# Kernel tuning notes

Hardware: AMD Instinct MI355X
Metric: run time of the kernel (lower is better)

Reference implementation:

```python
import jax, jax.numpy as jnp
import numpy as np
from jax import lax

R = 2            # search_range
S = 2 * R + 1    # window extent per axis
NCH = S ** 3     # output channels (125)


def _offset_table():
    # Loop order matches the original triple loop (i over H, j over W, h over D).
    # Channel index (S*i + S*j + h) may be negative -> Python negative indexing,
    starts, chans = [], []
    for i in range(-R, R + 1):          # H shift
        for j in range(-R, R + 1):      # W shift
            for h in range(-R, R + 1):  # D shift
                # out[a] = sum_c x1[a] * x2[a - shift]; padded start = R - shift
                starts.append((R - h, R - i, R - j))
                chans.append((S * i + S * j + h) % NCH)
    src = np.full(NCH, -1, dtype=np.int64)
    for t, c in enumerate(chans):
        src[c] = t
    return np.asarray(starts, np.int32), src


def setup_inputs() -> dict:
    key = jax.random.key(0)
    k1, k2 = jax.random.split(key)
    B, C, D, H, W = 2, 64, 32, 64, 64
    x1 = jax.random.normal(k1, (B, C, D, H, W), dtype=jnp.float32)
    x2 = jax.random.normal(k2, (B, C, D, H, W), dtype=jnp.float32)
    return {"x1": x1, "x2": x2}


def reference(x1, x2):
    B, C, D, H, W = x1.shape
    starts_np, src_np = _offset_table()
    starts = jnp.asarray(starts_np)                          # [NCH, 3]
    # zero-pad x2 so every shifted window is a static-size slice
    x2p = jnp.pad(x2, ((0, 0), (0, 0), (R, R), (R, R), (R, R)))

    def corr(off):
        x2s = lax.dynamic_slice(x2p, (0, 0, off[0], off[1], off[2]),
                                (B, C, D, H, W))
        return jnp.einsum('bcdhw,bcdhw->bdhw', x1, x2s)

    corrs = lax.map(corr, starts)                            # [NCH, B, D, H, W]
    src = jnp.asarray(src_np)
    written = (src >= 0)[:, None, None, None, None]
    cv = jnp.where(written, corrs[jnp.clip(src, 0)], jnp.float32(0.0))
    return jnp.transpose(cv, (1, 0, 2, 3, 4)) / NCH          # [B, NCH, D, H, W]
```

## Files before the change

kernel.cpp:

```cpp
#include <hip/hip_runtime.h>

#define B_ 2
#define C_ 64
#define D_ 32
#define H_ 64
#define W_ 64
#define NCH 125
#define HW_ 4096
#define DHW_ 131072
#define CDHW_ 8388608

#define TROWS 8
#define TBUF (TROWS * W_)
#define WREG (3 * TBUF)

__device__ __attribute__((aligned(16))) const float g_zero[4] = {0.f, 0.f, 0.f, 0.f};

__device__ __forceinline__ void glds16(const float* g, float* l) {
    __builtin_amdgcn_global_load_lds(
        (const __attribute__((address_space(1))) void*)g,
        (__attribute__((address_space(3))) void*)l, 16, 0, 0);
}

__global__ __launch_bounds__(128, 5) void cv_all(const float* __restrict__ x1,
                                                 const float* __restrict__ x2,
                                                 float* __restrict__ out)
{
    __shared__ __align__(16) float lds[4 + 2 * WREG + 4];

    const int tid  = threadIdx.y * 16 + threadIdx.x;
    const int lane = tid & 63;
    const int w    = tid >> 6;
    const int tx   = lane & 15;
    const int lr0  = lane >> 4;

    const int lin     = blockIdx.x;
    const int logical = (lin & 7) * 320 + (lin >> 3);
    const int bz   = logical % 10;
    const int rest = logical / 10;
    const int y0   = (rest & 7) * 8;
    const int d    = rest >> 3;
    const int b    = bz / 5;
    const int hi   = bz - b * 5;
    const int hh   = hi - 2;
    const int y0w  = y0 + 4 * w;
    const int y    = y0w + lr0;
    const int x    = tx * 4;
    const int zd   = d - hh;
    const bool zok = (zd >= 0) && (zd < D_);

    const float* x2b = x2 + (size_t)b * CDHW_ + (size_t)(zok ? zd : 0) * HW_;
    const int q   = lane & 15;
    const int grA = y0w - 2 + (lane >> 4);
    const int grB = y0w + 2 + (lane >> 4);
    const bool vA = zok && (grA >= 0);
    const bool vB = zok && (grB < H_);
    const float* pA = vA ? (x2b + grA * W_ + 4 * q) : g_zero;
    const float* pB = vB ? (x2b + grB * W_ + 4 * q) : g_zero;
    const int sA = vA ? DHW_ : 0;
    const int sB = vB ? DHW_ : 0;

    const int wbase = 4 + w * WREG;
    const float* p1 = x1 + (size_t)b * CDHW_ + (size_t)d * HW_ + (y * W_ + x);

    float* obz = out + (size_t)b * NCH * DHW_ + (size_t)(23 + hi * 16) * DHW_
                     + (size_t)d * HW_ + (y * W_ + x);
    const float4 zero4 = make_float4(0.f, 0.f, 0.f, 0.f);

    glds16(pA, lds + wbase);
    glds16(pB, lds + wbase + TBUF / 2);
    float4 a0 = *(const float4*)p1;
    pA += sA; pB += sB;

    float acc[9][4];
#pragma unroll
    for (int k = 0; k < 9; ++k)
#pragma unroll
        for (int j = 0; j < 4; ++j) acc[k][j] = 0.f;

    const bool lo_edge = (tx == 0);
    const bool hi_edge = (tx == 15);

#pragma unroll 2
    for (int c = 0; c < C_; ++c) {
        float* dst = lds + wbase + ((c + 1) % 3) * TBUF;
        glds16(pA, dst);
        glds16(pB, dst + TBUF / 2);
        float4 a1 = *(const float4*)(p1 + (size_t)((c + 1) & 63) * DHW_);
        if (c < 62) { pA += sA; pB += sB; }

        asm volatile("s_waitcnt vmcnt(3)" ::: "memory");

        const float* Bb = lds + wbase + (c % 3) * TBUF;
        const float4 a = a0;
        float2 k0A, k0B;
#pragma unroll
        for (int k = 0; k < 5; ++k) {
            const float* pr = Bb + (lr0 + k) * W_ + x;
            const float2 cA = *(const float2*)(pr + 2);
            float2 cB = *(const float2*)(pr + 4);
            cB.x = hi_edge ? 0.f : cB.x;
            cB.y = hi_edge ? 0.f : cB.y;
            if (k == 0) { k0A = cA; k0B = cB; }
            const int ai = 4 - k;
            acc[ai][0] += a.x * cA.x;
            acc[ai][1] += a.y * cA.y;
            acc[ai][2] += a.z * cB.x;
            acc[ai][3] += a.w * cB.y;
        }
        {
            const float* pr = Bb + lr0 * W_ + x;
            float2 rlA = *(const float2*)(pr - 2);
            const float2 rlB = *(const float2*)(pr);
            rlA.x = lo_edge ? 0.f : rlA.x;
            rlA.y = lo_edge ? 0.f : rlA.y;
            const float r8[8] = {rlA.x, rlA.y, rlB.x, rlB.y,
                                 k0A.x, k0A.y, k0B.x, k0B.y};
#pragma unroll
            for (int s = 1; s <= 4; ++s) {
                const int ai = s + 4;
                acc[ai][0] += a.x * r8[4 - s];
                acc[ai][1] += a.y * r8[5 - s];
                acc[ai][2] += a.z * r8[6 - s];
                acc[ai][3] += a.w * r8[7 - s];
            }
        }
        a0 = a1;

        if ((c & 3) == 0)
            *(float4*)(obz + (size_t)(c >> 2) * DHW_) = zero4;
    }

    float* ob = out + (size_t)b * NCH * DHW_ + (size_t)d * HW_ + (y * W_ + x);
    const float inv = 1.0f / 125.0f;
#pragma unroll
    for (int k = 0; k < 9; ++k) {
        const int s = k - 4;
        int ch = 5 * s + hh;
        ch = (ch % NCH + NCH) % NCH;
        float4 v;
        v.x = acc[k][0] * inv;
        v.y = acc[k][1] * inv;
        v.z = acc[k][2] * inv;
        v.w = acc[k][3] * inv;
        *(float4*)(ob + (size_t)ch * DHW_) = v;
    }
}

extern "C" void kernel_launch(void* const* d_in, const int* in_sizes, int n_in,
                              void* d_out, int out_size, void* d_ws, size_t ws_size,
                              hipStream_t stream) {
    const float* x1 = (const float*)d_in[0];
    const float* x2 = (const float*)d_in[1];
    float* out = (float*)d_out;
    cv_all<<<dim3(2560, 1, 1), dim3(16, 8, 1), 0, stream>>>(x1, x2, out);
}
```

Before: 269.4 us.

## Replace direct global-to-LDS loads with register-staged double-buffered padded LDS tiles

```diff
diff --git a/kernel.cpp b/kernel.cpp
--- a/kernel.cpp
+++ b/kernel.cpp
@@ -10,23 +10,22 @@
 #define DHW_ 131072
 #define CDHW_ 8388608
 
-#define TROWS 8
-#define TBUF (TROWS * W_)
-#define WREG (3 * TBUF)
+#define RSTRIDE 65
+#define TBUF (8 * RSTRIDE)
+#define WREG (2 * TBUF)
 
 __device__ __attribute__((aligned(16))) const float g_zero[4] = {0.f, 0.f, 0.f, 0.f};
 
-__device__ __forceinline__ void glds16(const float* g, float* l) {
-    __builtin_amdgcn_global_load_lds(
-        (const __attribute__((address_space(1))) void*)g,
-        (__attribute__((address_space(3))) void*)l, 16, 0, 0);
+__device__ __forceinline__ void lds_fence() {
+    asm volatile("s_waitcnt lgkmcnt(0)" ::: "memory");
+    __builtin_amdgcn_sched_barrier(0);
 }
 
 __global__ __launch_bounds__(128, 5) void cv_all(const float* __restrict__ x1,
                                                  const float* __restrict__ x2,
                                                  float* __restrict__ out)
 {
-    __shared__ __align__(16) float lds[4 + 2 * WREG + 4];
+    __shared__ __align__(16) float lds[4 + WREG + 4 + WREG + 4];
 
     const int tid  = threadIdx.y * 16 + threadIdx.x;
     const int lane = tid & 63;
@@ -50,9 +49,9 @@
     const bool zok = (zd >= 0) && (zd < D_);
 
     const float* x2b = x2 + (size_t)b * CDHW_ + (size_t)(zok ? zd : 0) * HW_;
-    const int q   = lane & 15;
-    const int grA = y0w - 2 + (lane >> 4);
-    const int grB = y0w + 2 + (lane >> 4);
+    const int q   = tx;
+    const int grA = y0w - 2 + lr0;
+    const int grB = y0w + 2 + lr0;
     const bool vA = zok && (grA >= 0);
     const bool vB = zok && (grB < H_);
     const float* pA = vA ? (x2b + grA * W_ + 4 * q) : g_zero;
@@ -60,17 +59,34 @@
     const int sA = vA ? DHW_ : 0;
     const int sB = vB ? DHW_ : 0;
 
-    const int wbase = 4 + w * WREG;
+    const int wbase = 4 + w * (WREG + 4);
+    const int woA   = RSTRIDE * lr0 + 4 * q;
+    const int woB   = woA + 4 * RSTRIDE;
+    const int rdb   = RSTRIDE * lr0 + x;
+
     const float* p1 = x1 + (size_t)b * CDHW_ + (size_t)d * HW_ + (y * W_ + x);
 
     float* obz = out + (size_t)b * NCH * DHW_ + (size_t)(23 + hi * 16) * DHW_
                      + (size_t)d * HW_ + (y * W_ + x);
     const float4 zero4 = make_float4(0.f, 0.f, 0.f, 0.f);
 
-    glds16(pA, lds + wbase);
-    glds16(pB, lds + wbase + TBUF / 2);
-    float4 a0 = *(const float4*)p1;
+    float4 vA0 = *(const float4*)pA;
+    float4 vB0 = *(const float4*)pB;
+    float4 a0  = *(const float4*)p1;
     pA += sA; pB += sB;
+    float4 rA1 = *(const float4*)pA;
+    float4 rB1 = *(const float4*)pB;
+    float4 a1  = *(const float4*)(p1 + DHW_);
+    pA += sA; pB += sB;
+
+    {
+        float* w0 = lds + wbase;
+        w0[woA + 0] = vA0.x; w0[woA + 1] = vA0.y;
+        w0[woA + 2] = vA0.z; w0[woA + 3] = vA0.w;
+        w0[woB + 0] = vB0.x; w0[woB + 1] = vB0.y;
+        w0[woB + 2] = vB0.z; w0[woB + 3] = vB0.w;
+    }
+    lds_fence();
 
     float acc[9][4];
 #pragma unroll
@@ -83,39 +99,38 @@
 
 #pragma unroll 2
     for (int c = 0; c < C_; ++c) {
-        float* dst = lds + wbase + ((c + 1) % 3) * TBUF;
-        glds16(pA, dst);
-        glds16(pB, dst + TBUF / 2);
-        float4 a1 = *(const float4*)(p1 + (size_t)((c + 1) & 63) * DHW_);
-        if (c < 62) { pA += sA; pB += sB; }
+        float4 nA = *(const float4*)pA;
+        float4 nB = *(const float4*)pB;
+        float4 na = *(const float4*)(p1 + (size_t)((c + 2) & 63) * DHW_);
+        if (c < 61) { pA += sA; pB += sB; }
 
-        asm volatile("s_waitcnt vmcnt(3)" ::: "memory");
-
-        const float* Bb = lds + wbase + (c % 3) * TBUF;
+        const float* Bb = lds + wbase + (c & 1) * TBUF + rdb;
         const float4 a = a0;
-        float2 k0A, k0B;
+        float k0A0, k0A1, k0B0, k0B1;
 #pragma unroll
         for (int k = 0; k < 5; ++k) {
-            const float* pr = Bb + (lr0 + k) * W_ + x;
-            const float2 cA = *(const float2*)(pr + 2);
-            float2 cB = *(const float2*)(pr + 4);
-            cB.x = hi_edge ? 0.f : cB.x;
-            cB.y = hi_edge ? 0.f : cB.y;
-            if (k == 0) { k0A = cA; k0B = cB; }
+            const int ro = RSTRIDE * k;
+            const float cA0 = Bb[ro + 2];
+            const float cA1 = Bb[ro + 3];
+            float cB0 = Bb[ro + 4];
+            float cB1 = Bb[ro + 5];
+            cB0 = hi_edge ? 0.f : cB0;
+            cB1 = hi_edge ? 0.f : cB1;
+            if (k == 0) { k0A0 = cA0; k0A1 = cA1; k0B0 = cB0; k0B1 = cB1; }
             const int ai = 4 - k;
-            acc[ai][0] += a.x * cA.x;
-            acc[ai][1] += a.y * cA.y;
-            acc[ai][2] += a.z * cB.x;
-            acc[ai][3] += a.w * cB.y;
+            acc[ai][0] += a.x * cA0;
+            acc[ai][1] += a.y * cA1;
+            acc[ai][2] += a.z * cB0;
+            acc[ai][3] += a.w * cB1;
         }
         {
-            const float* pr = Bb + lr0 * W_ + x;
-            float2 rlA = *(const float2*)(pr - 2);
-            const float2 rlB = *(const float2*)(pr);
-            rlA.x = lo_edge ? 0.f : rlA.x;
-            rlA.y = lo_edge ? 0.f : rlA.y;
-            const float r8[8] = {rlA.x, rlA.y, rlB.x, rlB.y,
-                                 k0A.x, k0A.y, k0B.x, k0B.y};
+            float rl0 = Bb[-2];
+            float rl1 = Bb[-1];
+            const float rl2 = Bb[0];
+            const float rl3 = Bb[1];
+            rl0 = lo_edge ? 0.f : rl0;
+            rl1 = lo_edge ? 0.f : rl1;
+            const float r8[8] = {rl0, rl1, rl2, rl3, k0A0, k0A1, k0B0, k0B1};
 #pragma unroll
             for (int s = 1; s <= 4; ++s) {
                 const int ai = s + 4;
@@ -125,7 +140,18 @@
                 acc[ai][3] += a.w * r8[7 - s];
             }
         }
-        a0 = a1;
+
+        {
+            float* wd = lds + wbase + ((c + 1) & 1) * TBUF;
+            wd[woA + 0] = rA1.x; wd[woA + 1] = rA1.y;
+            wd[woA + 2] = rA1.z; wd[woA + 3] = rA1.w;
+            wd[woB + 0] = rB1.x; wd[woB + 1] = rB1.y;
+            wd[woB + 2] = rB1.z; wd[woB + 3] = rB1.w;
+        }
+        lds_fence();
+
+        rA1 = nA; rB1 = nB;
+        a0 = a1; a1 = na;
 
         if ((c & 3) == 0)
             *(float4*)(obz + (size_t)(c >> 2) * DHW_) = zero4;
```

Measured after the change: 375.6 us. 39.4% more time.
